# Kernel optimization log

Measured on AMD Instinct MI355X. Metric: run time of the kernel, lower is better.

The kernel has to match this reference:

```python
import jax, jax.numpy as jnp
import numpy as np

DIM = 768
NUM_HEADS = 12
HEAD_DIM = DIM // NUM_HEADS


def setup_inputs() -> dict:
    key = jax.random.key(0)
    k0, k1, k2 = jax.random.split(key, 3)
    B, N = 8, 1024
    x = jax.random.normal(k0, (B, N, DIM), dtype=jnp.float32)
    w_qkv = jax.random.normal(k1, (DIM, 3 * DIM), dtype=jnp.float32) * (DIM ** -0.5)
    b_qkv = jnp.zeros((3 * DIM,), dtype=jnp.float32)
    w_proj = jax.random.normal(k2, (DIM, DIM), dtype=jnp.float32) * (DIM ** -0.5)
    b_proj = jnp.zeros((DIM,), dtype=jnp.float32)
    return {"x": x, "w_qkv": w_qkv, "b_qkv": b_qkv, "w_proj": w_proj, "b_proj": b_proj}


def reference(x, w_qkv, b_qkv, w_proj, b_proj):
    B, N, C = x.shape
    scale = HEAD_DIM ** -0.5
    qkv = x @ w_qkv + b_qkv                                  # [B, N, 3*C]
    qkv = qkv.reshape(B, N, 3, NUM_HEADS, HEAD_DIM).transpose(2, 0, 3, 1, 4)
    q, k, v = qkv[0], qkv[1], qkv[2]                          # each [B, H, N, hd]
    attn = jnp.einsum('bhqd,bhkd->bhqk', q, k) * scale        # [B, H, N, N]
    attn = jax.nn.softmax(attn, axis=-1)
    out = jnp.einsum('bhqk,bhkd->bhqd', attn, v)              # [B, H, N, hd]
    out = out.transpose(0, 2, 1, 3).reshape(B, N, C)
    return out @ w_proj + b_proj
```

## Files before the change

### kernel.cpp

```cpp
#include <hip/hip_runtime.h>
#include <cstdint>
#include <cmath>

#define B_ 8
#define S_ 1024
#define D_ 768
#define H_ 12
#define HD_ 64

typedef __bf16 bf16;
typedef __attribute__((ext_vector_type(8))) __bf16 bf16x8;
typedef __attribute__((ext_vector_type(4))) float floatx4;

typedef const __attribute__((address_space(1))) unsigned int* gas_ptr;
typedef __attribute__((address_space(3))) unsigned int* las_ptr;

__device__ __forceinline__ void async_ld16(const void* g, void* l) {
    gas_ptr gp = (gas_ptr)(uintptr_t)g;
    las_ptr lp = (las_ptr)(unsigned)(uintptr_t)l;
    __builtin_amdgcn_global_load_lds(gp, lp, 16, 0, 0);
}

__device__ __forceinline__ void xcd_swizzle(int& bx, int& by) {
    const int nx = gridDim.x, ny = gridDim.y;
    const int lin = blockIdx.y * nx + blockIdx.x;
    const int xcd = lin & 7;
    const int loc = lin >> 3;
    by = xcd * (ny >> 3) + loc / nx;
    bx = loc % nx;
}

__device__ __forceinline__ void stage32(const bf16* __restrict__ A,
                                        const bf16* __restrict__ Bt,
                                        long m0, long n0, long K, int kb,
                                        bf16* Asb, bf16* Bsb, int tid) {
#pragma unroll
    for (int r = 0; r < 2; r++) {
        const int idx = r * 256 + tid;
        const int rr  = idx >> 2;
        const int kc  = (idx & 3) * 8;
        async_ld16(A  + (m0 + rr) * K + kb + kc, (char*)Asb + idx * 16);
        async_ld16(Bt + (n0 + rr) * K + kb + kc, (char*)Bsb + idx * 16);
    }
}

__device__ __forceinline__ void transpose_dev(const float* __restrict__ in,
                                              bf16* __restrict__ out,
                                              int N, int K, int n0, int k0,
                                              bf16 (*tile)[66], int tid) {
#pragma unroll
    for (int r = 0; r < 4; r++) {
        int idx = r * 256 + tid;
        int row = idx >> 4;
        int c0  = (idx & 15) * 4;
        float4 v = *(const float4*)(in + (size_t)(k0 + row) * N + n0 + c0);
        tile[c0 + 0][row] = (bf16)v.x;
        tile[c0 + 1][row] = (bf16)v.y;
        tile[c0 + 2][row] = (bf16)v.z;
        tile[c0 + 3][row] = (bf16)v.w;
    }
    __syncthreads();
#pragma unroll
    for (int r = 0; r < 2; r++) {
        int idx = r * 256 + tid;
        int orow = idx >> 3;
        int kk   = (idx & 7) * 8;
        union { bf16x8 v; bf16 e[8]; } u;
#pragma unroll
        for (int j = 0; j < 8; j++) u.e[j] = tile[orow][kk + j];
        *(bf16x8*)(out + (size_t)(n0 + orow) * K + k0 + kk) = u.v;
    }
}

__global__ __launch_bounds__(256) void prep_all(
    const float* __restrict__ x, const float* __restrict__ w_qkv,
    const float* __restrict__ w_proj,
    bf16* __restrict__ xb, bf16* __restrict__ wqkvt, bf16* __restrict__ wprojt)
{
    __shared__ bf16 tile[64][66];
    const int blk = blockIdx.x, tid = threadIdx.x;
    if (blk < 6144) {
        int i = (blk * 256 + tid) * 4;
        float4 v = *(const float4*)(x + i);
        xb[i]     = (bf16)v.x;
        xb[i + 1] = (bf16)v.y;
        xb[i + 2] = (bf16)v.z;
        xb[i + 3] = (bf16)v.w;
    } else if (blk < 6576) {
        int t = blk - 6144;
        transpose_dev(w_qkv, wqkvt, 2304, 768, (t % 36) * 64, (t / 36) * 64, tile, tid);
    } else {
        int t = blk - 6576;
        transpose_dev(w_proj, wprojt, 768, 768, (t % 12) * 64, (t / 12) * 64, tile, tid);
    }
}

__global__ void transpose_v(const bf16* __restrict__ vbuf, bf16* __restrict__ vt) {
    __shared__ bf16 tile[64][66];
    const int tid = threadIdx.x;
    const int kt = blockIdx.x, h = blockIdx.y, b = blockIdx.z;
    const bf16* src = vbuf + ((size_t)b * S_ + (size_t)kt * 64) * D_ + h * 64;
#pragma unroll
    for (int r = 0; r < 2; r++) {
        int idx = r * 256 + tid;
        int kr = idx >> 3;
        int d0 = (idx & 7) * 8;
        bf16x8 v = *(const bf16x8*)(src + (size_t)kr * D_ + d0);
#pragma unroll
        for (int j = 0; j < 8; j++) {
            int p  = d0 + j;
            int dt = (p >> 2) + 16 * (p & 3);
            tile[dt][kr] = v[j];
        }
    }
    __syncthreads();
    bf16* dst = vt + ((size_t)(b * H_ + h) * 64) * 1024 + kt * 64;
#pragma unroll
    for (int r = 0; r < 2; r++) {
        int idx = r * 256 + tid;
        int dr = idx >> 3;
        int k0 = (idx & 7) * 8;
        union { bf16x8 v; bf16 e[8]; } u;
#pragma unroll
        for (int j = 0; j < 8; j++) {
            int kp  = k0 + j;
            int grp = kp & 32;
            int w32 = kp & 31;
            int gg  = w32 >> 3;
            int jj  = w32 & 7;
            int tk  = grp + ((jj < 4) ? (4 * gg + jj) : (16 + 4 * gg + jj - 4));
            u.e[j] = tile[dr][tk];
        }
        *(bf16x8*)(dst + (size_t)dr * 1024 + k0) = u.v;
    }
}

__global__ __launch_bounds__(256, 2) void gemm_qkv(
    const bf16* __restrict__ A, const bf16* __restrict__ Bt,
    const float* __restrict__ bias,
    bf16* __restrict__ qpack, bf16* __restrict__ kpack, bf16* __restrict__ vbuf)
{
    __shared__ __align__(16) bf16 As[2][128 * 32];
    __shared__ __align__(16) bf16 Bs[2][128 * 32];
    const int N = 2304, K = 768;
    const int NKT = K / 32;

    const int tid  = threadIdx.x;
    const int lane = tid & 63;
    const int w    = tid >> 6;
    const int wm   = (w >> 1) * 64;
    const int wn   = (w & 1) * 64;
    int bx, by;
    xcd_swizzle(bx, by);
    const long m0  = (long)by * 128;
    const long n0  = (long)bx * 128;
    const int c    = lane & 15;
    const int g    = lane >> 4;

    const floatx4 fzero = {0.f, 0.f, 0.f, 0.f};
    floatx4 acc[4][4];
#pragma unroll
    for (int i = 0; i < 4; i++)
#pragma unroll
        for (int j = 0; j < 4; j++) acc[i][j] = fzero;

    stage32(A, Bt, m0, n0, K, 0, As[0], Bs[0], tid);
    __syncthreads();

    for (int kt = 0; kt < NKT; kt++) {
        const int cur = kt & 1;
        if (kt + 1 < NKT)
            stage32(A, Bt, m0, n0, K, (kt + 1) * 32, As[cur ^ 1], Bs[cur ^ 1], tid);

        bf16x8 af[4], bfr[4];
#pragma unroll
        for (int i = 0; i < 4; i++) {
            af[i]  = *(const bf16x8*)(As[cur] + (wm + i * 16 + c) * 32 + g * 8);
            bfr[i] = *(const bf16x8*)(Bs[cur] + (wn + i * 16 + c) * 32 + g * 8);
        }
#pragma unroll
        for (int i = 0; i < 4; i++)
#pragma unroll
            for (int j = 0; j < 4; j++)
                acc[i][j] = __builtin_amdgcn_mfma_f32_16x16x32_bf16(af[i], bfr[j], acc[i][j], 0, 0, 0);

        __syncthreads();
    }

    const int head = (int)((n0 + wn) >> 6);
    const int rm   = wm + g * 4;
    float bv[4];
#pragma unroll
    for (int j = 0; j < 4; j++) bv[j] = bias[(int)n0 + wn + c + 16 * j];
    const int bb    = (int)(m0 >> 10);
    const int sbase = ((int)m0 & 1023) + rm;

    if (head < 24) {
        const float sc = (head < 12) ? 0.125f : 1.0f;
        bf16* dst = ((head < 12) ? qpack : kpack)
                  + (((size_t)((bb * H_ + (head < 12 ? head : head - 12)) * 1024 + sbase)) << 6)
                  + 4 * c;
#pragma unroll
        for (int i = 0; i < 4; i++)
#pragma unroll
            for (int e = 0; e < 4; e++) {
                union { bf16 h4[4]; uint64_t u; } pk;
#pragma unroll
                for (int j = 0; j < 4; j++) pk.h4[j] = (bf16)((acc[i][j][e] + bv[j]) * sc);
                *(uint64_t*)(dst + (size_t)(i * 16 + e) * 64) = pk.u;
            }
    } else {
        bf16* dst = vbuf + ((size_t)(bb * 1024 + sbase)) * 768 + (head - 24) * 64 + 4 * c;
#pragma unroll
        for (int i = 0; i < 4; i++)
#pragma unroll
            for (int e = 0; e < 4; e++) {
                union { bf16 h4[4]; uint64_t u; } pk;
#pragma unroll
                for (int j = 0; j < 4; j++) pk.h4[j] = (bf16)(acc[i][j][e] + bv[j]);
                *(uint64_t*)(dst + (size_t)(i * 16 + e) * 768) = pk.u;
            }
    }
}

__global__ __launch_bounds__(256, 2) void gemm_bt(
    const bf16* __restrict__ A, const bf16* __restrict__ Bt,
    const float* __restrict__ bias, float* __restrict__ C,
    int M, int N, int K)
{
    __shared__ __align__(16) bf16 As[2][128 * 32];
    __shared__ __align__(16) bf16 Bs[2][128 * 32];

    const int tid  = threadIdx.x;
    const int lane = tid & 63;
    const int w    = tid >> 6;
    const int wm   = (w >> 1) * 64;
    const int wn   = (w & 1) * 64;
    int bx, by;
    xcd_swizzle(bx, by);
    const long m0  = (long)by * 128;
    const long n0  = (long)bx * 128;
    const int c    = lane & 15;
    const int g    = lane >> 4;
    const int NKT  = K / 32;

    const floatx4 fzero = {0.f, 0.f, 0.f, 0.f};
    floatx4 acc[4][4];
#pragma unroll
    for (int i = 0; i < 4; i++)
#pragma unroll
        for (int j = 0; j < 4; j++) acc[i][j] = fzero;

    stage32(A, Bt, m0, n0, K, 0, As[0], Bs[0], tid);
    __syncthreads();

    for (int kt = 0; kt < NKT; kt++) {
        const int cur = kt & 1;
        if (kt + 1 < NKT)
            stage32(A, Bt, m0, n0, K, (kt + 1) * 32, As[cur ^ 1], Bs[cur ^ 1], tid);

        bf16x8 af[4], bfr[4];
#pragma unroll
        for (int i = 0; i < 4; i++) {
            af[i]  = *(const bf16x8*)(As[cur] + (wm + i * 16 + c) * 32 + g * 8);
            bfr[i] = *(const bf16x8*)(Bs[cur] + (wn + i * 16 + c) * 32 + g * 8);
        }
#pragma unroll
        for (int i = 0; i < 4; i++)
#pragma unroll
            for (int j = 0; j < 4; j++)
                acc[i][j] = __builtin_amdgcn_mfma_f32_16x16x32_bf16(af[i], bfr[j], acc[i][j], 0, 0, 0);

        __syncthreads();
    }

    const int cn = wn + c;
    const int rm = wm + g * 4;
#pragma unroll
    for (int j = 0; j < 4; j++) {
        const long gn = n0 + cn + j * 16;
        const float bv = bias[gn];
#pragma unroll
        for (int i = 0; i < 4; i++) {
            const long gm = m0 + rm + i * 16;
#pragma unroll
            for (int e = 0; e < 4; e++)
                C[(gm + e) * (long)N + gn] = acc[i][j][e] + bv;
        }
    }
}

__global__ __launch_bounds__(128, 3) void attn_fused(
    const bf16* __restrict__ qpack, const bf16* __restrict__ kpack,
    const bf16* __restrict__ vt, bf16* __restrict__ outp)
{
    __shared__ __align__(16) bf16 Ks[2048];
    __shared__ __align__(16) bf16 Vs[2048];

    const int tid  = threadIdx.x;
    const int lane = tid & 63;
    const int w    = tid >> 6;
    const int g    = lane >> 4;
    const int c    = lane & 15;

    const int id = blockIdx.x;
    const int bh = id % 96;
    const int qt = id / 96;
    const int h  = bh >> 3;
    const int b  = bh & 7;
    const int q0 = qt * 64 + w * 32;
    const bf16* qpb = qpack + ((size_t)(b * H_ + h) * 1024) * 64;
    const bf16* kpb = kpack + ((size_t)(b * H_ + h) * 1024) * 64;
    const bf16* vtb = vt    + ((size_t)(b * H_ + h) * 64) * 1024;

    bf16x8 qf[2][2];
#pragma unroll
    for (int qb = 0; qb < 2; qb++)
#pragma unroll
        for (int dc = 0; dc < 2; dc++)
            qf[qb][dc] = *(const bf16x8*)(qpb + (size_t)(q0 + qb * 16 + c) * 64 + dc * 32 + g * 8);

    union { uint32_t u[4]; bf16x8 v; } onesu;
    onesu.u[0] = onesu.u[1] = onesu.u[2] = onesu.u[3] = 0x3F803F80u;
    const bf16x8 onesf = onesu.v;

    const floatx4 fzero = {0.f, 0.f, 0.f, 0.f};
    floatx4 oacc[2][4];
    floatx4 lacc[2];
#pragma unroll
    for (int qb = 0; qb < 2; qb++) {
        lacc[qb] = fzero;
#pragma unroll
        for (int db = 0; db < 4; db++) oacc[qb][db] = fzero;
    }

    for (int kt = 0; kt < 32; kt++) {
        const int kg = kt * 32;
        __syncthreads();
#pragma unroll
        for (int r = 0; r < 2; r++) {
            const int i  = r * 128 + tid;
            const int dc = i >> 7, key = (i >> 2) & 31, dch = i & 3;
            async_ld16(kpb + (size_t)(kg + key) * 64 + dc * 32 + dch * 8, (char*)Ks + i * 16);
        }
#pragma unroll
        for (int r = 0; r < 2; r++) {
            const int i = r * 128 + tid;
            const int d = i >> 2, kch = i & 3;
            async_ld16(vtb + (size_t)d * 1024 + kg + kch * 8, (char*)Vs + i * 16);
        }
        __syncthreads();

        bf16x8 kf[2][2];
#pragma unroll
        for (int kb = 0; kb < 2; kb++)
#pragma unroll
            for (int dc = 0; dc < 2; dc++)
                kf[kb][dc] = *(const bf16x8*)(Ks + (dc * 32 + kb * 16 + c) * 32 + g * 8);

        bf16x8 vf[4];
#pragma unroll
        for (int db = 0; db < 4; db++)
            vf[db] = *(const bf16x8*)(Vs + (db * 16 + c) * 32 + g * 8);

#pragma unroll
        for (int qb = 0; qb < 2; qb++) {
            floatx4 s0 = fzero, s1 = fzero;
#pragma unroll
            for (int dc = 0; dc < 2; dc++) {
                s0 = __builtin_amdgcn_mfma_f32_16x16x32_bf16(kf[0][dc], qf[qb][dc], s0, 0, 0, 0);
                s1 = __builtin_amdgcn_mfma_f32_16x16x32_bf16(kf[1][dc], qf[qb][dc], s1, 0, 0, 0);
            }
            union { bf16 e[8]; bf16x8 v; } pa;
#pragma unroll
            for (int e4 = 0; e4 < 4; e4++) {
                pa.e[e4]     = (bf16)__expf(s0[e4]);
                pa.e[e4 + 4] = (bf16)__expf(s1[e4]);
            }
            lacc[qb] = __builtin_amdgcn_mfma_f32_16x16x32_bf16(onesf, pa.v, lacc[qb], 0, 0, 0);
#pragma unroll
            for (int db = 0; db < 4; db++)
                oacc[qb][db] = __builtin_amdgcn_mfma_f32_16x16x32_bf16(vf[db], pa.v, oacc[qb][db], 0, 0, 0);
        }
    }

#pragma unroll
    for (int qb = 0; qb < 2; qb++) {
        const float linv = 1.0f / lacc[qb][0];
        bf16* orow = outp + ((size_t)b * S_ + q0 + qb * 16 + c) * D_ + h * 64;
#pragma unroll
        for (int db = 0; db < 4; db++)
#pragma unroll
            for (int f = 0; f < 2; f++) {
                union { bf16 hh[2]; uint32_t u; } pk_;
                pk_.hh[0] = (bf16)(oacc[qb][db][2 * f]     * linv);
                pk_.hh[1] = (bf16)(oacc[qb][db][2 * f + 1] * linv);
                *(uint32_t*)(orow + db * 16 + 4 * g + 2 * f) = pk_.u;
            }
    }
}

extern "C" void kernel_launch(void* const* d_in, const int* in_sizes, int n_in,
                              void* d_out, int out_size, void* d_ws, size_t ws_size,
                              hipStream_t stream) {
    const float* x      = (const float*)d_in[0];
    const float* w_qkv  = (const float*)d_in[1];
    const float* b_qkv  = (const float*)d_in[2];
    const float* w_proj = (const float*)d_in[3];
    const float* b_proj = (const float*)d_in[4];
    float* out = (float*)d_out;

    bf16* xb     = (bf16*)d_ws;
    bf16* wqkvt  = xb     + (size_t)8192 * 768;
    bf16* wprojt = wqkvt  + (size_t)2304 * 768;
    bf16* qpack  = wprojt + (size_t)768 * 768;
    bf16* kpack  = qpack  + (size_t)96 * 1024 * 64;
    bf16* vbuf   = kpack  + (size_t)96 * 1024 * 64;
    bf16* vt     = vbuf   + (size_t)8192 * 768;
    bf16* attnb  = xb;

    prep_all<<<6720, 256, 0, stream>>>(x, w_qkv, w_proj, xb, wqkvt, wprojt);
    gemm_qkv<<<dim3(18, 64), 256, 0, stream>>>(xb, wqkvt, b_qkv, qpack, kpack, vbuf);
    transpose_v<<<dim3(16, 12, 8), 256, 0, stream>>>(vbuf, vt);
    attn_fused<<<1536, 128, 0, stream>>>(qpack, kpack, vt, attnb);
    gemm_bt<<<dim3(6, 64), 256, 0, stream>>>(attnb, wprojt, b_proj, out, 8192, 768, 768);
}
```

Measured before the change: 190.8 us.

## Deepen GEMM shared-memory pipeline to four stages with two-tile prefetch

Both GEMM kernels (QKV projection and output projection) move from a double-buffered LDS pipeline to a four-buffer ring that prefetches two K-tiles ahead. Explicit vmcnt waits and a single s_barrier per iteration replace the two __syncthreads, so async global-to-LDS loads can overlap more MFMA work. LDS use doubles to 64KB per block, which may limit occupancy against the 2-blocks-per-CU launch bound. Correctness now depends on the hardcoded vmcnt counts matching the number of loads issued by stage32.

```diff
diff --git a/kernel.cpp b/kernel.cpp
--- a/kernel.cpp
+++ b/kernel.cpp
@@ -140,8 +140,8 @@
     const float* __restrict__ bias,
     bf16* __restrict__ qpack, bf16* __restrict__ kpack, bf16* __restrict__ vbuf)
 {
-    __shared__ __align__(16) bf16 As[2][128 * 32];
-    __shared__ __align__(16) bf16 Bs[2][128 * 32];
+    __shared__ __align__(16) bf16 As[4][128 * 32];
+    __shared__ __align__(16) bf16 Bs[4][128 * 32];
     const int N = 2304, K = 768;
     const int NKT = K / 32;
 
@@ -164,27 +164,32 @@
 #pragma unroll
         for (int j = 0; j < 4; j++) acc[i][j] = fzero;
 
-    stage32(A, Bt, m0, n0, K, 0, As[0], Bs[0], tid);
-    __syncthreads();
+    stage32(A, Bt, m0, n0, K, 0,  As[0], Bs[0], tid);
+    stage32(A, Bt, m0, n0, K, 32, As[1], Bs[1], tid);
 
     for (int kt = 0; kt < NKT; kt++) {
-        const int cur = kt & 1;
-        if (kt + 1 < NKT)
-            stage32(A, Bt, m0, n0, K, (kt + 1) * 32, As[cur ^ 1], Bs[cur ^ 1], tid);
+        const int cb = kt & 3;
+        if (kt + 2 < NKT) {
+            stage32(A, Bt, m0, n0, K, (kt + 2) * 32, As[(kt + 2) & 3], Bs[(kt + 2) & 3], tid);
+            asm volatile("s_waitcnt vmcnt(8)" ::: "memory");
+        } else if (kt + 1 < NKT) {
+            asm volatile("s_waitcnt vmcnt(4)" ::: "memory");
+        } else {
+            asm volatile("s_waitcnt vmcnt(0)" ::: "memory");
+        }
+        __builtin_amdgcn_s_barrier();
 
         bf16x8 af[4], bfr[4];
 #pragma unroll
         for (int i = 0; i < 4; i++) {
-            af[i]  = *(const bf16x8*)(As[cur] + (wm + i * 16 + c) * 32 + g * 8);
-            bfr[i] = *(const bf16x8*)(Bs[cur] + (wn + i * 16 + c) * 32 + g * 8);
+            af[i]  = *(const bf16x8*)(As[cb] + (wm + i * 16 + c) * 32 + g * 8);
+            bfr[i] = *(const bf16x8*)(Bs[cb] + (wn + i * 16 + c) * 32 + g * 8);
         }
 #pragma unroll
         for (int i = 0; i < 4; i++)
 #pragma unroll
             for (int j = 0; j < 4; j++)
                 acc[i][j] = __builtin_amdgcn_mfma_f32_16x16x32_bf16(af[i], bfr[j], acc[i][j], 0, 0, 0);
-
-        __syncthreads();
     }
 
     const int head = (int)((n0 + wn) >> 6);
@@ -228,8 +233,8 @@
     const float* __restrict__ bias, float* __restrict__ C,
     int M, int N, int K)
 {
-    __shared__ __align__(16) bf16 As[2][128 * 32];
-    __shared__ __align__(16) bf16 Bs[2][128 * 32];
+    __shared__ __align__(16) bf16 As[4][128 * 32];
+    __shared__ __align__(16) bf16 Bs[4][128 * 32];
 
     const int tid  = threadIdx.x;
     const int lane = tid & 63;
@@ -251,27 +256,32 @@
 #pragma unroll
         for (int j = 0; j < 4; j++) acc[i][j] = fzero;
 
-    stage32(A, Bt, m0, n0, K, 0, As[0], Bs[0], tid);
-    __syncthreads();
+    stage32(A, Bt, m0, n0, K, 0,  As[0], Bs[0], tid);
+    stage32(A, Bt, m0, n0, K, 32, As[1], Bs[1], tid);
 
     for (int kt = 0; kt < NKT; kt++) {
-        const int cur = kt & 1;
-        if (kt + 1 < NKT)
-            stage32(A, Bt, m0, n0, K, (kt + 1) * 32, As[cur ^ 1], Bs[cur ^ 1], tid);
+        const int cb = kt & 3;
+        if (kt + 2 < NKT) {
+            stage32(A, Bt, m0, n0, K, (kt + 2) * 32, As[(kt + 2) & 3], Bs[(kt + 2) & 3], tid);
+            asm volatile("s_waitcnt vmcnt(8)" ::: "memory");
+        } else if (kt + 1 < NKT) {
+            asm volatile("s_waitcnt vmcnt(4)" ::: "memory");
+        } else {
+            asm volatile("s_waitcnt vmcnt(0)" ::: "memory");
+        }
+        __builtin_amdgcn_s_barrier();
 
         bf16x8 af[4], bfr[4];
 #pragma unroll
         for (int i = 0; i < 4; i++) {
-            af[i]  = *(const bf16x8*)(As[cur] + (wm + i * 16 + c) * 32 + g * 8);
-            bfr[i] = *(const bf16x8*)(Bs[cur] + (wn + i * 16 + c) * 32 + g * 8);
+            af[i]  = *(const bf16x8*)(As[cb] + (wm + i * 16 + c) * 32 + g * 8);
+            bfr[i] = *(const bf16x8*)(Bs[cb] + (wn + i * 16 + c) * 32 + g * 8);
         }
 #pragma unroll
         for (int i = 0; i < 4; i++)
 #pragma unroll
             for (int j = 0; j < 4; j++)
                 acc[i][j] = __builtin_amdgcn_mfma_f32_16x16x32_bf16(af[i], bfr[j], acc[i][j], 0, 0, 0);
-
-        __syncthreads();
     }
 
     const int cn = wn + c;
```

New measurement: 189.8 us. Within noise of the previous version (-0.5%).
